# Kernel tuning notes

Measured on AMD Instinct MI355X. Metric: run time of the kernel, lower is better.

## Reference

```python
import jax, jax.numpy as jnp
import numpy as np

# module hyperparameters (init_kwargs)
SLEN = 208          # full image side length in pixels
PTILE = 8           # padded tile side length
STEP = 2            # tile stride
EDGE = 3            # edge padding; tile interior = PTILE - 2*EDGE = 2 = STEP
MAXDET = 2          # max detections kept per tile


def _tile_coords():
    # replicates _get_tile_coords: coords[i] = [i // ny * step, i % ny * step]
    n = (SLEN - PTILE) // STEP + 1
    i = np.arange(n * n)
    coords = np.stack([(i // n) * STEP, (i % n) * STEP], axis=1).astype(np.float32)
    return jnp.asarray(coords)  # (P, 2)


def setup_inputs() -> dict:
    key = jax.random.key(0)
    k1, k2 = jax.random.split(key)
    locs = jax.random.uniform(k1, (16, 100, 2), dtype=jnp.float32)    # in [0,1)
    fluxes = jax.random.uniform(k2, (16, 100, 5), dtype=jnp.float32)
    return {"locs": locs, "fluxes": fluxes}


def reference(locs, fluxes):
    # Faithful translation of _get_params_in_tiles(tile_coords, max_detections,
    # slen, edge_padding, ptile_slen, locs, fluxes).
    tc = _tile_coords()                     # (P, 2)
    B, S, _ = locs.shape
    P = tc.shape[0]

    locs_pix = locs * (SLEN - 1)            # (B, S, 2) pixel coords
    left = tc + EDGE - 0.5                  # (P, 2)
    right = tc - 0.5 + PTILE - EDGE         # (P, 2)

    lp = locs_pix[:, None, :, :]            # (B, 1, S, 2)
    on2 = (lp > left[None, :, None, :]) & (lp < right[None, :, None, :]) & (lp != 0.0)
    is_on = (on2[..., 0] & on2[..., 1]).astype(jnp.float32)   # (B, P, S)
    is_on_flat = is_on.reshape(B * P, S)
    tile_n_sources = is_on_flat.sum(axis=1).astype(jnp.int64) if False else is_on_flat.sum(axis=1).astype(jnp.int32)

    # masked per-tile locations, shifted to tile-local coords, scaled, relu'd
    scale = PTILE - 2 * EDGE
    tile_locs = is_on[..., None] * locs_pix[:, None, :, :]     # (B, P, S, 2)
    tile_locs = (tile_locs - left[None, :, None, :]) / scale
    tile_locs = jax.nn.relu(tile_locs).reshape(B * P, S, 2)

    # front-sort: on-entries first (jax argsort is stable)
    idx = jnp.argsort(-is_on_flat.astype(jnp.int32), axis=1)   # (B*P, S)
    tile_locs = jnp.take_along_axis(tile_locs, idx[..., None], axis=1)

    # masked + gathered per-tile params (fluxes)
    tile_fluxes = (is_on[..., None] * fluxes[:, None, :, :]).reshape(B * P, S, -1)
    tile_fluxes = jnp.take_along_axis(tile_fluxes, idx[..., None], axis=1)

    tile_is_on = jnp.take_along_axis(is_on_flat, idx, axis=1)  # (B*P, S)

    # clip to max_detections
    tile_n_sources = jnp.minimum(tile_n_sources, MAXDET)
    return (tile_n_sources,
            tile_locs[:, :MAXDET],
            tile_fluxes[:, :MAXDET],
            tile_is_on[:, :MAXDET])
```

## Files before the change

kernel.cpp:

```cpp
#include <hip/hip_runtime.h>

#define NT     101
#define PTILES (NT * NT)
#define BATCH  16
#define NSRC   100
#define NTILES (BATCH * PTILES)
#define PBLK   256
#define NBLKX  ((PTILES + PBLK - 1) / PBLK)


__global__ __launch_bounds__(256)
void ImageEncoder_41944650613092_kernel(const float* __restrict__ locs,
                                        const float* __restrict__ fluxes,
                                        float* __restrict__ out)
{
    __shared__ __align__(16) int   s_t[NSRC];
    __shared__ float s_y[NSRC];
    __shared__ float s_x[NSRC];

    const int tid = threadIdx.x;
    const int b   = blockIdx.y;
    const int p   = blockIdx.x * PBLK + tid;

    if (tid < NSRC) {
        const float2 yx = ((const float2*)(locs + b * (NSRC * 2)))[tid];
        const float yp = yx.x * 207.0f;
        const float xp = yx.y * 207.0f;
        int r = (int)floorf((yp - 2.5f) * 0.5f);
        int c = (int)floorf((xp - 2.5f) * 0.5f);
        bool ok = (r >= 0) & (r < NT) & (c >= 0) & (c < NT);
        if (ok) {
            const float ly = (float)(2 * r) + 2.5f;
            const float lx = (float)(2 * c) + 2.5f;
            ok = (yp > ly) & (yp < ly + 2.0f) & (xp > lx) & (xp < lx + 2.0f);
        }
        s_t[tid] = ok ? (r * NT + c) : -1;
        s_y[tid] = yp;
        s_x[tid] = xp;
    }
    __syncthreads();

    if (p >= PTILES) return;
    const int t = b * PTILES + p;

    int cnt = 0, s0 = -1, s1 = -1;
    #pragma unroll
    for (int s4 = 0; s4 < NSRC; s4 += 4) {
        const int4 tq = *(const int4*)&s_t[s4];
        #pragma unroll
        for (int j = 0; j < 4; ++j) {
            const int tc = (j == 0) ? tq.x : (j == 1) ? tq.y : (j == 2) ? tq.z : tq.w;
            const bool m = (tc == p);
            if (m) {
                if (cnt == 0)      s0 = s4 + j;
                else if (cnt == 1) s1 = s4 + j;
                ++cnt;
            }
        }
    }

    float* out_n = out;
    float* out_l = out + NTILES;
    float* out_f = out + (size_t)NTILES * 5;
    float* out_o = out + (size_t)NTILES * 15;

    out_n[t] = fminf((float)cnt, 2.0f);

    float l4[4]   = {0.f, 0.f, 0.f, 0.f};
    float f10[10] = {0.f, 0.f, 0.f, 0.f, 0.f, 0.f, 0.f, 0.f, 0.f, 0.f};
    float o2[2]   = {0.f, 0.f};

    const int row = p / NT;
    const int col = p - row * NT;
    const float ly = (float)(2 * row) + 2.5f;
    const float lx = (float)(2 * col) + 2.5f;

    #pragma unroll
    for (int k = 0; k < 2; ++k) {
        const int s = (k == 0) ? s0 : s1;
        if (s >= 0) {
            l4[2 * k]     = (s_y[s] - ly) * 0.5f;
            l4[2 * k + 1] = (s_x[s] - lx) * 0.5f;
            const float* fb = fluxes + (size_t)(b * NSRC + s) * 5;
            #pragma unroll
            for (int j = 0; j < 5; ++j) f10[5 * k + j] = fb[j];
            o2[k] = 1.0f;
        }
    }

    *(float4*)(out_l + (size_t)t * 4) = make_float4(l4[0], l4[1], l4[2], l4[3]);
    #pragma unroll
    for (int j = 0; j < 5; ++j)
        *(float2*)(out_f + (size_t)t * 10 + 2 * j) = make_float2(f10[2 * j], f10[2 * j + 1]);
    *(float2*)(out_o + (size_t)t * 2) = make_float2(o2[0], o2[1]);
}

extern "C" void kernel_launch(void* const* d_in, const int* in_sizes, int n_in,
                              void* d_out, int out_size, void* d_ws, size_t ws_size,
                              hipStream_t stream) {
    const float* locs   = (const float*)d_in[0];
    const float* fluxes = (const float*)d_in[1];
    float* out = (float*)d_out;

    dim3 grid(NBLKX, BATCH);
    ImageEncoder_41944650613092_kernel<<<grid, 256, 0, stream>>>(locs, fluxes, out);
}
```

Measured before the change: 61.89 us.

## Compact block-local sources via ballot and stage flux output through LDS

Each block now compacts only the sources whose tile falls inside its 256-tile range, using wave ballots and popcount prefix positions, so per-thread scans loop over a short list instead of all 100 sources. The flux outputs are staged in shared memory and written back as contiguous float2 stores across the block, making global writes coalesced instead of strided by 40 bytes per thread. This costs extra barriers and about 10 KB of LDS per block, which may lower occupancy.

```diff
diff --git a/kernel.cpp b/kernel.cpp
--- a/kernel.cpp
+++ b/kernel.cpp
@@ -14,18 +14,25 @@
                                         const float* __restrict__ fluxes,
                                         float* __restrict__ out)
 {
-    __shared__ __align__(16) int   s_t[NSRC];
+    __shared__ int   s_cnt[2];
+    __shared__ int   s_tc[NSRC];
+    __shared__ int   s_id[NSRC];
     __shared__ float s_y[NSRC];
     __shared__ float s_x[NSRC];
+    __shared__ float s_f[PBLK * 10];
 
-    const int tid = threadIdx.x;
-    const int b   = blockIdx.y;
-    const int p   = blockIdx.x * PBLK + tid;
+    const int tid   = threadIdx.x;
+    const int b     = blockIdx.y;
+    const int pbase = blockIdx.x * PBLK;
+    const int p     = pbase + tid;
 
+    bool  m  = false;
+    int   tc = -1;
+    float yp = 0.f, xp = 0.f;
     if (tid < NSRC) {
         const float2 yx = ((const float2*)(locs + b * (NSRC * 2)))[tid];
-        const float yp = yx.x * 207.0f;
-        const float xp = yx.y * 207.0f;
+        yp = yx.x * 207.0f;
+        xp = yx.y * 207.0f;
         int r = (int)floorf((yp - 2.5f) * 0.5f);
         int c = (int)floorf((xp - 2.5f) * 0.5f);
         bool ok = (r >= 0) & (r < NT) & (c >= 0) & (c < NT);
@@ -34,37 +41,37 @@
             const float lx = (float)(2 * c) + 2.5f;
             ok = (yp > ly) & (yp < ly + 2.0f) & (xp > lx) & (xp < lx + 2.0f);
         }
-        s_t[tid] = ok ? (r * NT + c) : -1;
-        s_y[tid] = yp;
-        s_x[tid] = xp;
+        tc = r * NT + c;
+        m  = ok & (tc >= pbase) & (tc < pbase + PBLK);
+    }
+
+    int pos = 0;
+    if (tid < 128) {
+        const unsigned long long ball = __ballot(m);
+        const int lane = tid & 63;
+        const int wave = tid >> 6;
+        if (lane == 0) s_cnt[wave] = __popcll(ball);
+        pos = __popcll(ball & ((1ull << lane) - 1ull));
     }
     __syncthreads();
+    if (m) {
+        const int idx = ((tid >> 6) ? s_cnt[0] : 0) + pos;
+        s_tc[idx] = tc;
+        s_id[idx] = tid;
+        s_y[idx]  = yp;
+        s_x[idx]  = xp;
+    }
+    const int total = s_cnt[0] + s_cnt[1];
+    __syncthreads();
 
-    if (p >= PTILES) return;
-    const int t = b * PTILES + p;
-
-    int cnt = 0, s0 = -1, s1 = -1;
-    #pragma unroll
-    for (int s4 = 0; s4 < NSRC; s4 += 4) {
-        const int4 tq = *(const int4*)&s_t[s4];
-        #pragma unroll
-        for (int j = 0; j < 4; ++j) {
-            const int tc = (j == 0) ? tq.x : (j == 1) ? tq.y : (j == 2) ? tq.z : tq.w;
-            const bool m = (tc == p);
-            if (m) {
-                if (cnt == 0)      s0 = s4 + j;
-                else if (cnt == 1) s1 = s4 + j;
-                ++cnt;
-            }
+    int cnt = 0, i0 = -1, i1 = -1;
+    for (int i = 0; i < total; ++i) {
+        if (s_tc[i] == p) {
+            if (cnt == 0)      i0 = i;
+            else if (cnt == 1) i1 = i;
+            ++cnt;
         }
     }
-
-    float* out_n = out;
-    float* out_l = out + NTILES;
-    float* out_f = out + (size_t)NTILES * 5;
-    float* out_o = out + (size_t)NTILES * 15;
-
-    out_n[t] = fminf((float)cnt, 2.0f);
 
     float l4[4]   = {0.f, 0.f, 0.f, 0.f};
     float f10[10] = {0.f, 0.f, 0.f, 0.f, 0.f, 0.f, 0.f, 0.f, 0.f, 0.f};
@@ -77,22 +84,38 @@
 
     #pragma unroll
     for (int k = 0; k < 2; ++k) {
-        const int s = (k == 0) ? s0 : s1;
-        if (s >= 0) {
-            l4[2 * k]     = (s_y[s] - ly) * 0.5f;
-            l4[2 * k + 1] = (s_x[s] - lx) * 0.5f;
-            const float* fb = fluxes + (size_t)(b * NSRC + s) * 5;
+        const int i = (k == 0) ? i0 : i1;
+        if (i >= 0) {
+            l4[2 * k]     = (s_y[i] - ly) * 0.5f;
+            l4[2 * k + 1] = (s_x[i] - lx) * 0.5f;
+            const float* fb = fluxes + (size_t)(b * NSRC + s_id[i]) * 5;
             #pragma unroll
             for (int j = 0; j < 5; ++j) f10[5 * k + j] = fb[j];
             o2[k] = 1.0f;
         }
     }
 
-    *(float4*)(out_l + (size_t)t * 4) = make_float4(l4[0], l4[1], l4[2], l4[3]);
+    float* out_n = out;
+    float* out_l = out + NTILES;
+    float* out_f = out + (size_t)NTILES * 5;
+    float* out_o = out + (size_t)NTILES * 15;
+
+    const int t = b * PTILES + p;
+    if (p < PTILES) {
+        out_n[t] = fminf((float)cnt, 2.0f);
+        *(float4*)(out_l + (size_t)t * 4) = make_float4(l4[0], l4[1], l4[2], l4[3]);
+        *(float2*)(out_o + (size_t)t * 2) = make_float2(o2[0], o2[1]);
+    }
+
     #pragma unroll
-    for (int j = 0; j < 5; ++j)
-        *(float2*)(out_f + (size_t)t * 10 + 2 * j) = make_float2(f10[2 * j], f10[2 * j + 1]);
-    *(float2*)(out_o + (size_t)t * 2) = make_float2(o2[0], o2[1]);
+    for (int j = 0; j < 10; ++j) s_f[tid * 10 + j] = f10[j];
+    __syncthreads();
+
+    const int nvalid = min(PTILES - pbase, PBLK);
+    const int nfl2   = nvalid * 5;
+    float2* dst = (float2*)(out_f + ((size_t)b * PTILES + pbase) * 10);
+    const float2* src = (const float2*)s_f;
+    for (int i = tid; i < nfl2; i += PBLK) dst[i] = src[i];
 }
 
 extern "C" void kernel_launch(void* const* d_in, const int* in_sizes, int n_in,
```

Measured after the change: 60.00 us. 3.1% less time.
